# Performance work log

Hardware: AMD Instinct MI355X
Metric: run time of the kernel (lower is better)

## Reference

```python
import jax, jax.numpy as jnp
import numpy as np

N_E, E_DIM, BETA = 8192, 512, 0.25


def setup_inputs() -> dict:
    key = jax.random.key(0)
    k1, k2 = jax.random.split(key)
    z = jax.random.normal(k1, (16, 1024, E_DIM), dtype=jnp.float32)
    # embedding initialized uniform(-1/n_e, 1/n_e)
    emb_w = jax.random.uniform(k2, (N_E, E_DIM), dtype=jnp.float32,
                               minval=-1.0 / N_E, maxval=1.0 / N_E)
    return {"z": z, "emb_w": emb_w}


def reference(z, emb_w):
    B, T, D = z.shape
    zf = z.reshape(-1, D)  # [BT, D]
    # squared-distance matrix: ||z||^2 + ||e||^2 - 2 z e^T  -> [BT, n_e]
    d = (jnp.sum(zf * zf, axis=1, keepdims=True)
         + jnp.sum(emb_w * emb_w, axis=1)
         - 2.0 * jnp.einsum('bd,nd->bn', zf, emb_w))
    idx = jnp.argmin(d, axis=1)  # [BT]
    z_q = emb_w[idx].reshape(z.shape)  # [B, T, D]
    # legacy=False: beta * commit + codebook term
    loss = (BETA * jnp.mean((jax.lax.stop_gradient(z_q) - z) ** 2)
            + jnp.mean((z_q - jax.lax.stop_gradient(z)) ** 2))
    # straight-through: value equals z_q
    z_q_st = z + jax.lax.stop_gradient(z_q - z)
    idx_out = idx.reshape(B, T)
    v = jnp.var(idx_out.astype(jnp.float32))
    return z_q_st, loss, idx_out, v
```

## Files before the change

### kernel.cpp

```cpp
#include <hip/hip_runtime.h>


#define BT   16384
#define DIMS 512
#define NE   8192
#define NS   4
#define BN   256
#define NTPB (NE / NS / BN)
#define NSTEPS 64

#define LOSS_OFF 8388608
#define IDX_OFF  8388609
#define V_OFF    8404993

#define BEST_OFF  0
#define ENORM_OFF 131072
#define SUMS_OFF  163840
#define CNT_OFF   163864

typedef __attribute__((ext_vector_type(8))) short short8;
typedef __attribute__((ext_vector_type(4))) float floatx4;

#define AS1(p) ((const __attribute__((address_space(1))) void*)(p))
#define AS3(p) ((__attribute__((address_space(3))) void*)(p))

__device__ __forceinline__ unsigned f2bf(float f) {
    unsigned u = __builtin_bit_cast(unsigned, f);
    u += 0x7FFFu + ((u >> 16) & 1u);
    return u >> 16;
}

__global__ __launch_bounds__(256) void prep_kernel(
    const float* __restrict__ z, const float* __restrict__ emb,
    ushort* __restrict__ zh, ushort* __restrict__ ehh,
    float* __restrict__ enorm, unsigned long long* __restrict__ best,
    double* __restrict__ sums, unsigned* __restrict__ counter)
{
    const int lane = threadIdx.x & 63, w = threadIdx.x >> 6;
    const int b = blockIdx.x;
    if (b < NE / 4) {
        const int row = b * 4 + w;
        const float4* p = (const float4*)(emb + (size_t)row * DIMS + lane * 8);
        float4 a = p[0], bb = p[1];
        uint4 h;
        h.x = f2bf(a.x) | (f2bf(a.y) << 16);
        h.y = f2bf(a.z) | (f2bf(a.w) << 16);
        h.z = f2bf(bb.x) | (f2bf(bb.y) << 16);
        h.w = f2bf(bb.z) | (f2bf(bb.w) << 16);
        *(uint4*)(ehh + (size_t)row * DIMS + lane * 8) = h;
        float s = a.x*a.x + a.y*a.y + a.z*a.z + a.w*a.w
                + bb.x*bb.x + bb.y*bb.y + bb.z*bb.z + bb.w*bb.w;
        #pragma unroll
        for (int off = 32; off > 0; off >>= 1) s += __shfl_down(s, off, 64);
        if (lane == 0) enorm[row] = s;
    } else {
        const int row = (b - NE / 4) * 4 + w;
        const float4* p = (const float4*)(z + (size_t)row * DIMS + lane * 8);
        float4 a = p[0], bb = p[1];
        uint4 h;
        h.x = f2bf(a.x) | (f2bf(a.y) << 16);
        h.y = f2bf(a.z) | (f2bf(a.w) << 16);
        h.z = f2bf(bb.x) | (f2bf(bb.y) << 16);
        h.w = f2bf(bb.z) | (f2bf(bb.w) << 16);
        *(uint4*)(zh + (size_t)row * DIMS + lane * 8) = h;
    }
    const int gid = b * 256 + threadIdx.x;
    if (gid < BT) best[gid] = 0xFFFFFFFFFFFFFFFFULL;
    if (gid == 0) { sums[0] = 0.0; sums[1] = 0.0; sums[2] = 0.0; *counter = 0u; }
}


#define DSR8(dst, IDX) do {                                                    \
    unsigned addr_ = (unsigned)(size_t)AS3(&lds[IDX]);                         \
    asm volatile("ds_read_b128 %0, %1" : "=v"(dst) : "v"(addr_));              \
} while (0)

#define LGK(N_) do {                                                           \
    asm volatile("s_waitcnt lgkmcnt(" #N_ ")" ::: "memory");                   \
    __builtin_amdgcn_sched_barrier(0);                                         \
} while (0)

#define CL4(J_, BIDX_, KK_)                                                    \
    _Pragma("unroll")                                                          \
    for (int mi = 0; mi < 4; mi++)                                             \
        acc[mi][J_] = __builtin_amdgcn_mfma_f32_16x16x32_bf16(                 \
            a[mi][KK_], b[BIDX_], acc[mi][J_], 0, 0, 0);

#define STAGE_A(SA_, H_, DST_) do {                                            \
    const int sc_ = (SA_) & 63;                                                \
    const unsigned al_ = (DST_) + (unsigned)((((H_) * 128) + w * 8) * 64);     \
    const ushort* g_ = zA + (size_t)((H_) * 128) * DIMS + soff                 \
                     + ((sc_ & 7) * 64);                                       \
    __builtin_amdgcn_global_load_lds(AS1(g_), AS3(&lds[al_]), 16, 0, 0);       \
    __builtin_amdgcn_global_load_lds(AS1(g_ + (size_t)64 * DIMS),              \
                                     AS3(&lds[al_ + 4096]), 16, 0, 0);         \
} while (0)

#define STAGE_B(SB_, H_, DST_) do {                                            \
    const int sc_ = (SB_) & 63;                                                \
    const unsigned bl_ = (DST_) + (unsigned)((((H_) * 128) + w * 8) * 64);     \
    const ushort* g_ = eh + (size_t)(nsN + (sc_ >> 3) * 256 + (H_) * 128) * DIMS \
                     + soff + ((sc_ & 7) * 64);                                \
    __builtin_amdgcn_global_load_lds(AS1(g_), AS3(&lds[bl_]), 16, 0, 0);       \
    __builtin_amdgcn_global_load_lds(AS1(g_ + (size_t)64 * DIMS),              \
                                     AS3(&lds[bl_ + 4096]), 16, 0, 0);         \
} while (0)

#define STEP(S_, AR_, BR_, AW_, BW_, TM_) do {                                 \
    const int s_ = (S_);                                                       \
    short8 a[4][2], b[4];                                                      \
                                                                       \
    _Pragma("unroll") for (int mi = 0; mi < 4; mi++)                           \
        DSR8(a[mi][0], (AR_) + aro + mi * 1024 + pxo0);                        \
    _Pragma("unroll") for (int j = 0; j < 4; j++)                              \
        DSR8(b[j], (BR_) + bro + j * 1024 + pxo0);                             \
    STAGE_B(s_ + 1, 0, BW_); STAGE_B(s_ + 1, 1, BW_);                          \
    __builtin_amdgcn_s_setprio(1);                                             \
    LGK(3); CL4(0, 0, 0); LGK(2); CL4(1, 1, 0);                                \
    LGK(1); CL4(2, 2, 0); LGK(0); CL4(3, 3, 0);                                \
    __builtin_amdgcn_s_setprio(0);                                             \
                                                                       \
    _Pragma("unroll") for (int j = 0; j < 4; j++)                              \
        DSR8(b[j], (BR_) + bro + (4 + j) * 1024 + pxo0);                       \
    _Pragma("unroll") for (int mi = 0; mi < 4; mi++)                           \
        DSR8(a[mi][1], (AR_) + aro + mi * 1024 + pxo1);                        \
    STAGE_A(s_ + 2, 0, AW_); STAGE_A(s_ + 2, 1, AW_);                          \
    __builtin_amdgcn_s_setprio(1);                                             \
    LGK(7); CL4(4, 0, 0); LGK(6); CL4(5, 1, 0);                                \
    LGK(5); CL4(6, 2, 0); LGK(4); CL4(7, 3, 0);                                \
    __builtin_amdgcn_s_setprio(0);                                             \
                                                                       \
    _Pragma("unroll") for (int j = 0; j < 4; j++)                              \
        DSR8(b[j], (BR_) + bro + j * 1024 + pxo1);                             \
    __builtin_amdgcn_s_setprio(1);                                             \
    LGK(3); CL4(0, 0, 1); LGK(2); CL4(1, 1, 1);                                \
    LGK(1); CL4(2, 2, 1); LGK(0); CL4(3, 3, 1);                                \
    __builtin_amdgcn_s_setprio(0);                                             \
                                                                       \
    _Pragma("unroll") for (int j = 0; j < 4; j++)                              \
        DSR8(b[j], (BR_) + bro + (4 + j) * 1024 + pxo1);                       \
    __builtin_amdgcn_s_setprio(1);                                             \
    LGK(3); CL4(4, 0, 1); LGK(2); CL4(5, 1, 1);                                \
    LGK(1); CL4(6, 2, 1); LGK(0); CL4(7, 3, 1);                                \
    __builtin_amdgcn_s_setprio(0);                                             \
    __builtin_amdgcn_sched_barrier(0);                                         \
    if ((TM_) == 0) asm volatile("s_waitcnt vmcnt(4)" ::: "memory");           \
    __builtin_amdgcn_s_barrier();                                              \
} while (0)

__global__ __launch_bounds__(512, 2) void argmin_mfma(
    const ushort* __restrict__ zh, const ushort* __restrict__ eh,
    const float* __restrict__ enorm, unsigned long long* __restrict__ best)
{
    __shared__ __align__(16) ushort lds[81920];

    const int t = threadIdx.x;
    const int w = t >> 6, lane = t & 63;
    const int quad = lane >> 4, l15 = lane & 15;

    const int d = blockIdx.x;
    const int xcd = d & 7, slot = d >> 3;
    const int ns = xcd >> 1;
    const int mt = slot * 2 + (xcd & 1);
    const int m0 = mt * 256;
    const int nsN = ns * (NTPB * BN);

    const int wrow = (w & 3) * 64;
    const int wcol = (w >> 2) * 128;

    const int l8 = lane >> 3, c8 = lane & 7;
    const int chunk = c8 ^ l8;
    const int soff = (w * 8 + l8) * DIMS + chunk * 8;
    const ushort* zA = zh + (size_t)m0 * DIMS;
    const float* enormg = enorm + nsN;

    const int pxo0 = (quad ^ (l15 & 7)) * 8;
    const int pxo1 = ((4 + quad) ^ (l15 & 7)) * 8;
    const int aro = (wrow + l15) * 64;
    const int bro = (wcol + l15) * 64;

    floatx4 acc[4][8];
    #pragma unroll
    for (int mi = 0; mi < 4; mi++)
        #pragma unroll
        for (int nj = 0; nj < 8; nj++)
            acc[mi][nj] = (floatx4){0.f, 0.f, 0.f, 0.f};

    float bs[16];
    int   bn_[16];
    #pragma unroll
    for (int k = 0; k < 16; k++) { bs[k] = 3.4e38f; bn_[k] = 0; }

    STAGE_A(0, 0, 0u);     STAGE_A(0, 1, 0u);
    STAGE_B(0, 0, 49152u); STAGE_B(0, 1, 49152u);
    STAGE_A(1, 0, 16384u); STAGE_A(1, 1, 16384u);
    asm volatile("s_waitcnt vmcnt(4)" ::: "memory");
    __builtin_amdgcn_s_barrier();

    unsigned aR = 0u, aN = 16384u, aW = 32768u;

    for (int sp = 0; sp < NSTEPS; sp += 2) {
        STEP(sp, aR, 49152u, aW, 65536u, 0);
        { unsigned t_ = aR; aR = aN; aN = aW; aW = t_; }
        STEP(sp + 1, aR, 65536u, aW, 49152u, (sp == NSTEPS - 2) ? 2 : 0);
        { unsigned t_ = aR; aR = aN; aN = aW; aW = t_; }

        if ((sp & 7) == 6) {
            const int nt = sp >> 3;
            const int eb = nt * 256 + wcol + l15;
            const int nbase = nsN + eb;
            float en[8];
            #pragma unroll
            for (int nj = 0; nj < 8; nj++) {
                const float* ep_ = enormg + eb + nj * 16;
                asm volatile("global_load_dword %0, %1, off"
                             : "=v"(en[nj]) : "v"(ep_));
            }
            asm volatile("s_waitcnt vmcnt(0)" ::: "memory");
            __builtin_amdgcn_sched_barrier(0);
            #pragma unroll
            for (int nj = 0; nj < 8; nj++) {
                const int n = nbase + nj * 16;
                #pragma unroll
                for (int mi = 0; mi < 4; mi++) {
                    #pragma unroll
                    for (int r = 0; r < 4; r++) {
                        const int k = mi * 4 + r;
                        const float sc = fmaf(-2.0f, acc[mi][nj][r], en[nj]);
                        if (sc < bs[k]) { bs[k] = sc; bn_[k] = n; }
                    }
                    acc[mi][nj] = (floatx4){0.f, 0.f, 0.f, 0.f};
                }
            }
        }
    }

    asm volatile("s_waitcnt vmcnt(0)" ::: "memory");

    #pragma unroll
    for (int mi = 0; mi < 4; mi++)
        #pragma unroll
        for (int r = 0; r < 4; r++) {
            const int k = mi * 4 + r;
            unsigned su = __builtin_bit_cast(unsigned, bs[k]);
            su = (su & 0x80000000u) ? ~su : (su | 0x80000000u);
            unsigned long long key = ((unsigned long long)su << 32) | (unsigned)bn_[k];
            #pragma unroll
            for (int off = 1; off < 16; off <<= 1) {
                unsigned long long o = __shfl_xor(key, off, 64);
                key = (o < key) ? o : key;
            }
            if (l15 == 0) atomicMin(&best[m0 + wrow + mi * 16 + quad * 4 + r], key);
        }
}

__global__ __launch_bounds__(256) void gather_loss_kernel(
    const float* __restrict__ z, const float* __restrict__ emb,
    const unsigned long long* __restrict__ best,
    float* __restrict__ out, double* __restrict__ sums, unsigned* __restrict__ counter)
{
    __shared__ int sIdx[32];
    __shared__ double red[4];
    const int t = threadIdx.x;
    const int row0 = blockIdx.x * 32;
    double myIdxSum = 0.0, myIdxSq = 0.0;
    if (t < 32) {
        int row = row0 + t;
        int idx = (int)(unsigned)(best[row] & 0xFFFFFFFFULL);
        sIdx[t] = idx;
        out[IDX_OFF + row] = (float)idx;
        myIdxSum = (double)idx;
        myIdxSq = (double)idx * (double)idx;
    }
    __syncthreads();
    double acc = 0.0;
    #pragma unroll 4
    for (int i = 0; i < 16; i++) {
        int e = i * 1024 + t * 4;
        int rl = e >> 9;
        int c = e & 511;
        int idx = sIdx[rl];
        float4 zv = *(const float4*)(z + (size_t)(row0 + rl) * DIMS + c);
        float4 ev = *(const float4*)(emb + (size_t)idx * DIMS + c);
        *(float4*)(out + (size_t)(row0 + rl) * DIMS + c) = ev;
        float dx = zv.x - ev.x, dy = zv.y - ev.y;
        float dz = zv.z - ev.z, dw = zv.w - ev.w;
        acc += (double)(dx * dx + dy * dy) + (double)(dz * dz + dw * dw);
    }
    const int lane = t & 63, wv = t >> 6;
    #pragma unroll
    for (int off = 32; off > 0; off >>= 1) {
        acc      += __shfl_down(acc, off, 64);
        myIdxSum += __shfl_down(myIdxSum, off, 64);
        myIdxSq  += __shfl_down(myIdxSq, off, 64);
    }
    if (lane == 0) red[wv] = acc;
    __syncthreads();
    if (t == 0) {
        double tot = red[0] + red[1] + red[2] + red[3];
        atomicAdd(&sums[0], tot);
        atomicAdd(&sums[1], myIdxSum);
        atomicAdd(&sums[2], myIdxSq);
        __threadfence();
        unsigned old = atomicAdd(counter, 1u);
        if (old == gridDim.x - 1) {
            __threadfence();
            double s0 = atomicAdd(&sums[0], 0.0);
            double s1 = atomicAdd(&sums[1], 0.0);
            double s2 = atomicAdd(&sums[2], 0.0);
            out[LOSS_OFF] = (float)(1.25 * s0 / (double)((size_t)BT * DIMS));
            double m = s1 / (double)BT;
            out[V_OFF] = (float)(s2 / (double)BT - m * m);
        }
    }
}

extern "C" void kernel_launch(void* const* d_in, const int* in_sizes, int n_in,
                              void* d_out, int out_size, void* d_ws, size_t ws_size,
                              hipStream_t stream) {
    const float* z = (const float*)d_in[0];
    const float* emb = (const float*)d_in[1];
    float* out = (float*)d_out;
    char* ws = (char*)d_ws;
    unsigned long long* best = (unsigned long long*)(ws + BEST_OFF);
    float* enorm  = (float*)(ws + ENORM_OFF);
    double* sums  = (double*)(ws + SUMS_OFF);
    unsigned* counter = (unsigned*)(ws + CNT_OFF);

    ushort* zh = (ushort*)out;
    ushort* ehh = zh + (size_t)BT * DIMS;

    hipLaunchKernelGGL(prep_kernel, dim3(NE / 4 + BT / 4), dim3(256), 0, stream,
                       z, emb, zh, ehh, enorm, best, sums, counter);
    hipLaunchKernelGGL(argmin_mfma, dim3(256), dim3(512), 0, stream,
                       zh, ehh, enorm, best);
    hipLaunchKernelGGL(gather_loss_kernel, dim3(BT / 32), dim3(256), 0, stream,
                       z, emb, best, out, sums, counter);
}
```

Before: 253.5 us.

## Fuse gather and loss into argmin kernel via last-arriving-block epilogue

Moves the bf16 copies of z and the codebook into the workspace so the output buffer is free, then has the last of the four N-split blocks for each 256-row tile run the gather, write z_q, and accumulate loss and index statistics. A global tile counter lets the final tile finish the scalar outputs. This drops the separate gather_loss kernel launch and lets the epilogue overlap with other tiles' GEMM work. In exchange it adds threadfences and atomics, depends on the workspace being large enough, and leaves only 64 of 256 blocks doing the gather.

```diff
diff --git a/kernel.cpp b/kernel.cpp
--- a/kernel.cpp
+++ b/kernel.cpp
@@ -17,6 +17,10 @@
 #define ENORM_OFF 131072
 #define SUMS_OFF  163840
 #define CNT_OFF   163864
+#define TILE_OFF  163872
+#define ZH_OFF    165888
+#define EHH_OFF   (ZH_OFF + (size_t)BT * DIMS * 2)
+#define WS_NEED   (EHH_OFF + (size_t)NE * DIMS * 2)
 
 typedef __attribute__((ext_vector_type(8))) short short8;
 typedef __attribute__((ext_vector_type(4))) float floatx4;
@@ -34,7 +38,8 @@
     const float* __restrict__ z, const float* __restrict__ emb,
     ushort* __restrict__ zh, ushort* __restrict__ ehh,
     float* __restrict__ enorm, unsigned long long* __restrict__ best,
-    double* __restrict__ sums, unsigned* __restrict__ counter)
+    double* __restrict__ sums, unsigned* __restrict__ counter,
+    unsigned* __restrict__ tcnt, int fused)
 {
     const int lane = threadIdx.x & 63, w = threadIdx.x >> 6;
     const int b = blockIdx.x;
@@ -67,6 +72,7 @@
     const int gid = b * 256 + threadIdx.x;
     if (gid < BT) best[gid] = 0xFFFFFFFFFFFFFFFFULL;
     if (gid == 0) { sums[0] = 0.0; sums[1] = 0.0; sums[2] = 0.0; *counter = 0u; }
+    if (fused && gid < 65) tcnt[gid] = 0u;
 }
 
 
@@ -150,7 +156,10 @@
 
 __global__ __launch_bounds__(512, 2) void argmin_mfma(
     const ushort* __restrict__ zh, const ushort* __restrict__ eh,
-    const float* __restrict__ enorm, unsigned long long* __restrict__ best)
+    const float* __restrict__ enorm, unsigned long long* __restrict__ best,
+    const float* __restrict__ z, const float* __restrict__ emb,
+    float* __restrict__ out, double* __restrict__ sums,
+    unsigned* __restrict__ tcnt, int fused)
 {
     __shared__ __align__(16) ushort lds[81920];
 
@@ -252,6 +261,72 @@
             }
             if (l15 == 0) atomicMin(&best[m0 + wrow + mi * 16 + quad * 4 + r], key);
         }
+
+    if (!fused) return;
+
+    __threadfence();
+    __syncthreads();
+    volatile int* flg = (volatile int*)&lds[0];
+    if (t == 0) {
+        unsigned old = atomicAdd(&tcnt[mt], 1u);
+        *flg = (old == NS - 1) ? 1 : 0;
+    }
+    __syncthreads();
+    if (!*flg) return;
+    __threadfence();
+
+    int* sIdx = (int*)&lds[64];
+    double idxS = 0.0, idxQ = 0.0;
+    if (t < 256) {
+        const int row = m0 + t;
+        const int idx = (int)(unsigned)(best[row] & 0xFFFFFFFFULL);
+        sIdx[t] = idx;
+        out[IDX_OFF + row] = (float)idx;
+        idxS = (double)idx;
+        idxQ = (double)idx * (double)idx;
+    }
+    __syncthreads();
+    double accL = 0.0;
+    #pragma unroll 4
+    for (int i = 0; i < 64; i++) {
+        const int e4 = i * 512 + t;
+        const int rl = e4 >> 7;
+        const int c  = (e4 & 127) * 4;
+        const int idx = sIdx[rl];
+        const float4 zv = *(const float4*)(z + (size_t)(m0 + rl) * DIMS + c);
+        const float4 ev = *(const float4*)(emb + (size_t)idx * DIMS + c);
+        *(float4*)(out + (size_t)(m0 + rl) * DIMS + c) = ev;
+        const float dx = zv.x - ev.x, dy = zv.y - ev.y;
+        const float dz = zv.z - ev.z, dw = zv.w - ev.w;
+        accL += (double)(dx * dx + dy * dy) + (double)(dz * dz + dw * dw);
+    }
+    #pragma unroll
+    for (int off = 32; off > 0; off >>= 1) {
+        accL += __shfl_down(accL, off, 64);
+        idxS += __shfl_down(idxS, off, 64);
+        idxQ += __shfl_down(idxQ, off, 64);
+    }
+    double* red = (double*)&lds[1024];
+    if (lane == 0) { red[w] = accL; red[8 + w] = idxS; red[16 + w] = idxQ; }
+    __syncthreads();
+    if (t == 0) {
+        double s0 = 0.0, s1 = 0.0, s2 = 0.0;
+        for (int i = 0; i < 8; i++) { s0 += red[i]; s1 += red[8+i]; s2 += red[16+i]; }
+        atomicAdd(&sums[0], s0);
+        atomicAdd(&sums[1], s1);
+        atomicAdd(&sums[2], s2);
+        __threadfence();
+        unsigned old = atomicAdd(&tcnt[64], 1u);
+        if (old == 63u) {
+            __threadfence();
+            double t0 = atomicAdd(&sums[0], 0.0);
+            double t1 = atomicAdd(&sums[1], 0.0);
+            double t2 = atomicAdd(&sums[2], 0.0);
+            out[LOSS_OFF] = (float)(1.25 * t0 / (double)((size_t)BT * DIMS));
+            double mm = t1 / (double)BT;
+            out[V_OFF] = (float)(t2 / (double)BT - mm * mm);
+        }
+    }
 }
 
 __global__ __launch_bounds__(256) void gather_loss_kernel(
@@ -326,14 +401,19 @@
     float* enorm  = (float*)(ws + ENORM_OFF);
     double* sums  = (double*)(ws + SUMS_OFF);
     unsigned* counter = (unsigned*)(ws + CNT_OFF);
-
-    ushort* zh = (ushort*)out;
-    ushort* ehh = zh + (size_t)BT * DIMS;
+    unsigned* tcnt    = (unsigned*)(ws + TILE_OFF);
+
+    const int fused = (ws_size >= WS_NEED) ? 1 : 0;
+
+    ushort* zh  = fused ? (ushort*)(ws + ZH_OFF) : (ushort*)out;
+    ushort* ehh = fused ? (ushort*)(ws + EHH_OFF)
+                        : (ushort*)out + (size_t)BT * DIMS;
 
     hipLaunchKernelGGL(prep_kernel, dim3(NE / 4 + BT / 4), dim3(256), 0, stream,
-                       z, emb, zh, ehh, enorm, best, sums, counter);
+                       z, emb, zh, ehh, enorm, best, sums, counter, tcnt, fused);
     hipLaunchKernelGGL(argmin_mfma, dim3(256), dim3(512), 0, stream,
-                       zh, ehh, enorm, best);
-    hipLaunchKernelGGL(gather_loss_kernel, dim3(BT / 32), dim3(256), 0, stream,
-                       z, emb, best, out, sums, counter);
+                       zh, ehh, enorm, best, z, emb, out, sums, tcnt, fused);
+    if (!fused)
+        hipLaunchKernelGGL(gather_loss_kernel, dim3(BT / 32), dim3(256), 0, stream,
+                           z, emb, best, out, sums, counter);
 }
```

Result: slower. 294.9 us (+16.3%).
